# Kernel optimization log

Hardware: AMD Instinct MI355X
Metric: run time of the kernel (lower is better)

Reference implementation:

```python
import jax, jax.numpy as jnp
import numpy as np

B, N, C = 8, 4096, 768
H = 4 * C  # mlp hidden
EPS = 1e-7
LN_EPS = 1e-5


def _ln(x, g, b):
    mu = jnp.mean(x, axis=-1, keepdims=True)
    var = jnp.mean((x - mu) ** 2, axis=-1, keepdims=True)
    return (x - mu) * jax.lax.rsqrt(var + LN_EPS) * g + b


def _mlp(z, w1, b1, w2, b2):
    return jax.nn.gelu(z @ w1 + b1, approximate=False) @ w2 + b2


def setup_inputs() -> dict:
    key = jax.random.key(0)
    ks = jax.random.split(key, 16)
    s = 1.0 / np.sqrt(C)
    inp = {
        "x": jax.random.normal(ks[0], (B, N, C), jnp.float32),
        "y": jax.random.normal(ks[1], (B, N, C), jnp.float32),
        "mask": jax.random.randint(ks[2], (B, N, 1), 0, 2).astype(jnp.float32),
        "h": 64,
        "w": 64,
        "ln1_g": jnp.ones((C,), jnp.float32),
        "ln1_b": jnp.zeros((C,), jnp.float32),
        "Wq": jax.random.normal(ks[3], (C, C), jnp.float32) * s,
        "Wk": jax.random.normal(ks[4], (C, C), jnp.float32) * s,
        "Wv": jax.random.normal(ks[5], (C, C), jnp.float32) * s,
        "Wpx": jax.random.normal(ks[6], (2 * C, C), jnp.float32) * s,
        "Wpy": jax.random.normal(ks[7], (2 * C, C), jnp.float32) * s,
        "ln2_g": jnp.ones((C,), jnp.float32),
        "ln2_b": jnp.zeros((C,), jnp.float32),
        "fx1_w": jax.random.normal(ks[8], (C, H), jnp.float32) * s,
        "fx1_b": jnp.zeros((H,), jnp.float32),
        "fx2_w": jax.random.normal(ks[9], (H, C), jnp.float32) / np.sqrt(H),
        "fx2_b": jnp.zeros((C,), jnp.float32),
        "fy1_w": jax.random.normal(ks[10], (C, H), jnp.float32) * s,
        "fy1_b": jnp.zeros((H,), jnp.float32),
        "fy2_w": jax.random.normal(ks[11], (H, C), jnp.float32) / np.sqrt(H),
        "fy2_b": jnp.zeros((C,), jnp.float32),
    }
    return inp


def _minmax(s):
    mn = jnp.min(s, axis=1, keepdims=True)
    mx = jnp.max(s, axis=1, keepdims=True)
    return (s - mn) / (mx - mn + EPS)


def reference(x, y, mask, h, w, ln1_g, ln1_b, Wq, Wk, Wv, Wpx, Wpy,
              ln2_g, ln2_b, fx1_w, fx1_b, fx2_w, fx2_b, fy1_w, fy1_b, fy2_w, fy2_b):
    b, n, c = x.shape
    m = mask.reshape(b, n, 1)  # binary mask per token
    xn = _ln(x, ln1_g, ln1_b)
    yn = _ln(y, ln1_g, ln1_b)
    q = yn @ Wq  # (b,n,c)
    k = xn @ Wk
    v = xn @ Wv
    # masked GAP pools (Weighted_GAP): (b,c)
    fg = jnp.sum(q * m, axis=1) / (jnp.sum(m, axis=1) + 5e-4)
    bg = jnp.sum(q * (1.0 - m), axis=1) / (jnp.sum(1.0 - m, axis=1) + 5e-4)
    k_nrm = jnp.linalg.norm(k, axis=2)  # (b,n)
    fg_nrm = jnp.linalg.norm(fg, axis=1, keepdims=True)  # (b,1)
    bg_nrm = jnp.linalg.norm(bg, axis=1, keepdims=True)
    fg_s = jnp.einsum('bnc,bc->bn', k, fg) / (k_nrm * fg_nrm + EPS)
    bg_s = jnp.einsum('bnc,bc->bn', k, bg) / (k_nrm * bg_nrm + EPS)
    scores = _minmax(fg_s) - _minmax(bg_s)  # (b,n)
    pseudo_mask = scores.reshape(b, 1, h, w)
    attn = jax.nn.softmax(jnp.where(scores < 0, scores - 100.0, scores), axis=1)
    query_pro = jnp.einsum('bn,bnc->bc', attn, v)  # (b,c)
    qp_nrm = jnp.linalg.norm(query_pro, axis=1, keepdims=True)
    sim = jnp.sum(query_pro * fg, axis=1, keepdims=True) / (qp_nrm * fg_nrm + EPS)
    sim = (sim + 1.0) * 0.5  # (b,1)
    pro = sim * fg + (1.0 - sim) * query_pro  # (b,c)
    pro_b = jnp.broadcast_to(pro[:, None, :], x.shape)
    xo = x + jnp.concatenate([x, pro_b], axis=-1) @ Wpx
    yo = y + jnp.concatenate([y, pro_b], axis=-1) @ Wpy
    xo = xo + _mlp(_ln(xo, ln2_g, ln2_b), fx1_w, fx1_b, fx2_w, fx2_b)
    yo = yo + _mlp(_ln(yo, ln2_g, ln2_b), fy1_w, fy1_b, fy2_w, fy2_b)
    return (xo, yo, pseudo_mask)
```

## Files before the change

### kernel.cpp

```cpp
#include <hip/hip_runtime.h>
#include <math.h>

#define B_ 8
#define N_ 4096
#define C_ 768
#define H_ 3072
#define M_ (B_*N_)
#define NSPLIT 16

typedef unsigned short u16;
typedef unsigned int u32;
typedef __attribute__((ext_vector_type(8))) __bf16 bf16x8;
typedef __attribute__((ext_vector_type(4))) float f32x4;
typedef __attribute__((ext_vector_type(4))) unsigned short u16x4;
typedef __attribute__((ext_vector_type(8))) unsigned short u16x8;

__device__ __forceinline__ u16 f2bf(float f){
  u32 u = __float_as_uint(f);
  u32 r = (u + 0x7FFFu + ((u >> 16) & 1u)) >> 16;
  return (u16)r;
}
__device__ __forceinline__ float bf2f(u16 h){
  return __uint_as_float(((u32)h) << 16);
}
__device__ __forceinline__ void gload_lds16(const void* g, void* l){
  __builtin_amdgcn_global_load_lds((const __attribute__((address_space(1))) void*)g,
                                   (__attribute__((address_space(3))) void*)l, 16, 0, 0);
}

template<int EPI, int GM>
__global__ __launch_bounds__(512, 4) void gemm_bf16(
    const u16* __restrict__ A, const u16* __restrict__ BT,
    int K, int N, int NBN,
    void* __restrict__ outp,
    const float* __restrict__ resid,
    const float* __restrict__ rowv,
    const float* __restrict__ bias)
{
  __shared__ u16 lds[3][12288];
  const int tid = threadIdx.x;
  const int wid = tid >> 6, lane = tid & 63;

  const int nwg = gridDim.x;
  int wg = blockIdx.x;
  wg = (wg & 7) * (nwg >> 3) + (wg >> 3);
  const int GMN = GM * NBN;
  const int g = wg / GMN, r = wg % GMN;
  const int bm = (g*GM + (r % GM)) * 256;
  const int bn = (r / GM) * 128;

  const int wr = wid >> 1, wc = wid & 1;
  const int l15 = lane & 15;

  f32x4 acc[4][4];
#pragma unroll
  for (int i=0;i<4;i++)
#pragma unroll
    for (int j=0;j<4;j++) acc[i][j] = (f32x4){0.f,0.f,0.f,0.f};

  const int srow = tid >> 2;
  const int lchq = (tid & 3) ^ ((tid >> 3) & 3);
  const u16* agp0 = A  + (size_t)(bm + srow)*K       + lchq*8;
  const u16* agp1 = A  + (size_t)(bm + 128 + srow)*K + lchq*8;
  const u16* bgp0 = BT + (size_t)(bn + srow)*K       + lchq*8;

  auto STAGE = [&](int bi){
    char* base = (char*)lds[bi] + wid*1024;
    gload_lds16(agp0, base);
    gload_lds16(agp1, base + 8192);
    gload_lds16(bgp0, base + 16384);
    agp0 += 32; agp1 += 32; bgp0 += 32;
  };

  const int arow = wr*64 + l15;
  const int brow = wc*64 + l15;
  const int aswz = (arow >> 1) & 3;
  const int bswz = (brow >> 1) & 3;
  const int aoff = arow*32 + (((lane>>4) ^ aswz) << 3);
  const int boff = 8192 + brow*32 + (((lane>>4) ^ bswz) << 3);

  const int nk = K >> 5;
  STAGE(0);
  STAGE(1);
  int kk2 = 0;

#define KSTEP(BI) do {                                                        \
    if (kk2 == nk-1){ asm volatile("s_waitcnt vmcnt(0)" ::: "memory"); }      \
    else            { asm volatile("s_waitcnt vmcnt(3)" ::: "memory"); }      \
    __builtin_amdgcn_s_barrier();                                             \
    __builtin_amdgcn_sched_barrier(0);                                        \
    if (kk2+2 < nk) STAGE((BI)==0 ? 2 : (BI)-1);            \
    bf16x8 av[4], bv[4];                                                      \
    const u16* pa = &lds[BI][aoff];                                           \
    const u16* pb = &lds[BI][boff];                                           \
    _Pragma("unroll")                                                         \
    for (int i=0;i<4;i++){                                                    \
      av[i] = *reinterpret_cast<const bf16x8*>(pa + i*512);                   \
      bv[i] = *reinterpret_cast<const bf16x8*>(pb + i*512);                   \
    }                                                                         \
    _Pragma("unroll")                                                         \
    for (int i=0;i<4;i++)                                                     \
      _Pragma("unroll")                                                       \
      for (int j=0;j<4;j++)                                                   \
        acc[i][j] = __builtin_amdgcn_mfma_f32_16x16x32_bf16(av[i], bv[j],     \
                                                            acc[i][j],0,0,0); \
    kk2++;                                                                    \
  } while(0)

  for (int it = 0; it < nk/3; it++){
    KSTEP(0);
    KSTEP(1);
    KSTEP(2);
  }
#undef KSTEP

  const int col0 = bn + wc*64 + l15;
  const int row0 = bm + wr*64 + ((lane >> 4) << 2);
#pragma unroll
  for (int i=0;i<4;i++){
#pragma unroll
    for (int j=0;j<4;j++){
#pragma unroll
      for (int r2=0;r2<4;r2++){
        const int row = row0 + i*16 + r2;
        const int cj  = col0 + j*16;
        const size_t o = (size_t)row*N + cj;
        const float va = acc[i][j][r2];
        if constexpr (EPI == 0){
          ((u16*)outp)[o] = f2bf(va);
        } else if constexpr (EPI == 1){
          const float rs = __builtin_nontemporal_load(resid + o);
          ((float*)outp)[o] = rs + va + rowv[(row >> 12)*N + cj];
        } else if constexpr (EPI == 2){
          const float z = va + bias[cj];
          ((u16*)outp)[o] = f2bf(0.5f*z*(1.0f + erff(z*0.70710678f)));
        } else {
          float* po = (float*)outp + o;
          const float prev = __builtin_nontemporal_load(po);
          *po = prev + va + bias[cj];
        }
      }
    }
  }
}

__device__ __forceinline__ void ln_row(const float* __restrict__ p,
    const float* __restrict__ gam, const float* __restrict__ bet,
    u16* __restrict__ op, int lane)
{
  float4 v0 = *reinterpret_cast<const float4*>(p + lane*4);
  float4 v1 = *reinterpret_cast<const float4*>(p + lane*4 + 256);
  float4 v2 = *reinterpret_cast<const float4*>(p + lane*4 + 512);
  float s  = v0.x+v0.y+v0.z+v0.w + v1.x+v1.y+v1.z+v1.w + v2.x+v2.y+v2.z+v2.w;
  float sq = v0.x*v0.x+v0.y*v0.y+v0.z*v0.z+v0.w*v0.w
           + v1.x*v1.x+v1.y*v1.y+v1.z*v1.z+v1.w*v1.w
           + v2.x*v2.x+v2.y*v2.y+v2.z*v2.z+v2.w*v2.w;
#pragma unroll
  for (int o=32;o>0;o>>=1){ s += __shfl_xor(s,o); sq += __shfl_xor(sq,o); }
  const float mu = s * (1.f/C_);
  const float rs = rsqrtf(sq*(1.f/C_) - mu*mu + 1e-5f);
  float4 g0 = *reinterpret_cast<const float4*>(gam + lane*4);
  float4 g1 = *reinterpret_cast<const float4*>(gam + lane*4 + 256);
  float4 g2 = *reinterpret_cast<const float4*>(gam + lane*4 + 512);
  float4 b0 = *reinterpret_cast<const float4*>(bet + lane*4);
  float4 b1 = *reinterpret_cast<const float4*>(bet + lane*4 + 256);
  float4 b2 = *reinterpret_cast<const float4*>(bet + lane*4 + 512);
  u16x4 o0, o1, o2;
  o0[0]=f2bf((v0.x-mu)*rs*g0.x+b0.x); o0[1]=f2bf((v0.y-mu)*rs*g0.y+b0.y);
  o0[2]=f2bf((v0.z-mu)*rs*g0.z+b0.z); o0[3]=f2bf((v0.w-mu)*rs*g0.w+b0.w);
  o1[0]=f2bf((v1.x-mu)*rs*g1.x+b1.x); o1[1]=f2bf((v1.y-mu)*rs*g1.y+b1.y);
  o1[2]=f2bf((v1.z-mu)*rs*g1.z+b1.z); o1[3]=f2bf((v1.w-mu)*rs*g1.w+b1.w);
  o2[0]=f2bf((v2.x-mu)*rs*g2.x+b2.x); o2[1]=f2bf((v2.y-mu)*rs*g2.y+b2.y);
  o2[2]=f2bf((v2.z-mu)*rs*g2.z+b2.z); o2[3]=f2bf((v2.w-mu)*rs*g2.w+b2.w);
  *reinterpret_cast<u16x4*>(op + lane*4)       = o0;
  *reinterpret_cast<u16x4*>(op + lane*4 + 256) = o1;
  *reinterpret_cast<u16x4*>(op + lane*4 + 512) = o2;
}

__global__ __launch_bounds__(256) void ln_fwd(const float* __restrict__ in,
    const float* __restrict__ gam, const float* __restrict__ bet,
    u16* __restrict__ out)
{
  const int row  = blockIdx.x*4 + (threadIdx.x >> 6);
  const int lane = threadIdx.x & 63;
  ln_row(in + (size_t)row*C_, gam, bet, out + (size_t)row*C_, lane);
}

__global__ __launch_bounds__(256) void ln_fwd2(const float* __restrict__ inx,
    const float* __restrict__ iny, const float* __restrict__ gam,
    const float* __restrict__ bet, u16* __restrict__ outx, u16* __restrict__ outy,
    u16* __restrict__ outxb, u16* __restrict__ outyb)
{
  const int row  = blockIdx.x*4 + (threadIdx.x >> 6);
  const int lane = threadIdx.x & 63;
  const float* in = blockIdx.y ? iny : inx;
  u16* out  = blockIdx.y ? outy  : outx;
  u16* outb = blockIdx.y ? outyb : outxb;
  const float* p = in + (size_t)row*C_;
  u16* op  = out  + (size_t)row*C_;
  u16* opb = outb + (size_t)row*C_;

  float4 v0 = *reinterpret_cast<const float4*>(p + lane*4);
  float4 v1 = *reinterpret_cast<const float4*>(p + lane*4 + 256);
  float4 v2 = *reinterpret_cast<const float4*>(p + lane*4 + 512);
  u16x4 rb;
  rb[0]=f2bf(v0.x); rb[1]=f2bf(v0.y); rb[2]=f2bf(v0.z); rb[3]=f2bf(v0.w);
  *reinterpret_cast<u16x4*>(opb + lane*4) = rb;
  rb[0]=f2bf(v1.x); rb[1]=f2bf(v1.y); rb[2]=f2bf(v1.z); rb[3]=f2bf(v1.w);
  *reinterpret_cast<u16x4*>(opb + lane*4 + 256) = rb;
  rb[0]=f2bf(v2.x); rb[1]=f2bf(v2.y); rb[2]=f2bf(v2.z); rb[3]=f2bf(v2.w);
  *reinterpret_cast<u16x4*>(opb + lane*4 + 512) = rb;

  float s  = v0.x+v0.y+v0.z+v0.w + v1.x+v1.y+v1.z+v1.w + v2.x+v2.y+v2.z+v2.w;
  float sq = v0.x*v0.x+v0.y*v0.y+v0.z*v0.z+v0.w*v0.w
           + v1.x*v1.x+v1.y*v1.y+v1.z*v1.z+v1.w*v1.w
           + v2.x*v2.x+v2.y*v2.y+v2.z*v2.z+v2.w*v2.w;
#pragma unroll
  for (int o=32;o>0;o>>=1){ s += __shfl_xor(s,o); sq += __shfl_xor(sq,o); }
  const float mu = s * (1.f/C_);
  const float rs = rsqrtf(sq*(1.f/C_) - mu*mu + 1e-5f);
  float4 g0 = *reinterpret_cast<const float4*>(gam + lane*4);
  float4 g1 = *reinterpret_cast<const float4*>(gam + lane*4 + 256);
  float4 g2 = *reinterpret_cast<const float4*>(gam + lane*4 + 512);
  float4 b0 = *reinterpret_cast<const float4*>(bet + lane*4);
  float4 b1 = *reinterpret_cast<const float4*>(bet + lane*4 + 256);
  float4 b2 = *reinterpret_cast<const float4*>(bet + lane*4 + 512);
  u16x4 o0, o1, o2;
  o0[0]=f2bf((v0.x-mu)*rs*g0.x+b0.x); o0[1]=f2bf((v0.y-mu)*rs*g0.y+b0.y);
  o0[2]=f2bf((v0.z-mu)*rs*g0.z+b0.z); o0[3]=f2bf((v0.w-mu)*rs*g0.w+b0.w);
  o1[0]=f2bf((v1.x-mu)*rs*g1.x+b1.x); o1[1]=f2bf((v1.y-mu)*rs*g1.y+b1.y);
  o1[2]=f2bf((v1.z-mu)*rs*g1.z+b1.z); o1[3]=f2bf((v1.w-mu)*rs*g1.w+b1.w);
  o2[0]=f2bf((v2.x-mu)*rs*g2.x+b2.x); o2[1]=f2bf((v2.y-mu)*rs*g2.y+b2.y);
  o2[2]=f2bf((v2.z-mu)*rs*g2.z+b2.z); o2[3]=f2bf((v2.w-mu)*rs*g2.w+b2.w);
  *reinterpret_cast<u16x4*>(op + lane*4)       = o0;
  *reinterpret_cast<u16x4*>(op + lane*4 + 256) = o1;
  *reinterpret_cast<u16x4*>(op + lane*4 + 512) = o2;
}

__device__ __forceinline__ void tr_tile(const float* __restrict__ in,
    u16* __restrict__ outp, int R, int Cc, int t)
{
  __shared__ float tile[32][33];
  const int tilesx = Cc >> 5;
  const int c0 = (t % tilesx)*32, r0 = (t / tilesx)*32;
  const int tx = threadIdx.x & 31, ty = threadIdx.x >> 5;
#pragma unroll
  for (int i=0;i<32;i+=8)
    tile[ty+i][tx] = in[(size_t)(r0+ty+i)*Cc + c0+tx];
  __syncthreads();
#pragma unroll
  for (int i=0;i<32;i+=8)
    outp[(size_t)(c0+ty+i)*R + r0+tx] = f2bf(tile[tx][ty+i]);
}

__global__ __launch_bounds__(256) void transpose_all(
    const float* Wk, const float* Wpx, const float* Wpy,
    const float* f1x, const float* f2x, const float* f1y, const float* f2y,
    u16* WkT, u16* WpxT, u16* WpyT, u16* f1xT, u16* f2xT, u16* f1yT, u16* f2yT)
{
  int t = blockIdx.x;
  if (t < 1728){
    const int m = t / 576; t -= m*576;
    const float* in = (m==0)?Wk:((m==1)?Wpx:Wpy);
    u16* o = (m==0)?WkT:((m==1)?WpxT:WpyT);
    tr_tile(in, o, C_, C_, t);
  } else {
    t -= 1728;
    const int m = t / 2304; t -= m*2304;
    if (m==0)      tr_tile(f1x, f1xT, C_, H_, t);
    else if (m==1) tr_tile(f2x, f2xT, H_, C_, t);
    else if (m==2) tr_tile(f1y, f1yT, C_, H_, t);
    else           tr_tile(f2y, f2yT, H_, C_, t);
  }
}

__global__ __launch_bounds__(256) void pool_partial(const u16* __restrict__ q,
    const float* __restrict__ mask, float* __restrict__ pm, float* __restrict__ pa,
    float* __restrict__ mpart)
{
  const int c = blockIdx.x*256 + threadIdx.x;
  const int b = blockIdx.y, z = blockIdx.z;
  const int n0 = z*(N_/NSPLIT);
  const u16* qp = q + ((size_t)b*N_ + n0)*C_ + c;
  const float* mp = mask + (size_t)b*N_ + n0;
  float am=0.f, aa=0.f, ms=0.f;
  for (int n=0;n<N_/NSPLIT;n++){
    float v = bf2f(qp[(size_t)n*C_]);
    float m = mp[n];
    am += v*m; aa += v; ms += m;
  }
  const size_t o = ((size_t)z*B_ + b)*C_ + c;
  pm[o]=am; pa[o]=aa;
  if (blockIdx.x==0 && threadIdx.x==0) mpart[z*B_+b] = ms;
}

__global__ __launch_bounds__(256) void proto_fused(const float* __restrict__ pm,
    const float* __restrict__ pa, const float* __restrict__ mpart,
    const float* __restrict__ Wq,
    float* __restrict__ fg, float* __restrict__ bg,
    float* __restrict__ fgn, float* __restrict__ bgn)
{
  __shared__ float fin[C_], bin[C_];
  __shared__ float red[8];
  const int b = blockIdx.x, tid = threadIdx.x;
  float msum_b = 0.f;
#pragma unroll
  for (int z=0;z<NSPLIT;z++) msum_b += mpart[z*B_+b];
  for (int c=tid;c<C_;c+=256){
    float sm=0.f, sa=0.f;
#pragma unroll
    for (int z=0;z<NSPLIT;z++){ size_t o=((size_t)z*B_+b)*C_+c; sm+=pm[o]; sa+=pa[o]; }
    fin[c] = sm/(msum_b + 5e-4f);
    bin[c] = (sa - sm)/((float)N_ - msum_b + 5e-4f);
  }
  __syncthreads();
  const int j0 = tid, j1 = tid+256, j2 = tid+512;
  float f0=0,f1=0,f2=0,g0=0,g1=0,g2=0;
  for (int c=0;c<C_;c++){
    const float* w = Wq + (size_t)c*C_;
    float fc = fin[c], bc = bin[c];
    float w0=w[j0], w1=w[j1], w2=w[j2];
    f0 += fc*w0; f1 += fc*w1; f2 += fc*w2;
    g0 += bc*w0; g1 += bc*w1; g2 += bc*w2;
  }
  fg[b*C_+j0]=f0; fg[b*C_+j1]=f1; fg[b*C_+j2]=f2;
  bg[b*C_+j0]=g0; bg[b*C_+j1]=g1; bg[b*C_+j2]=g2;
  float sf = f0*f0+f1*f1+f2*f2, sb = g0*g0+g1*g1+g2*g2;
#pragma unroll
  for (int o=32;o>0;o>>=1){ sf+=__shfl_down(sf,o); sb+=__shfl_down(sb,o); }
  if ((tid&63)==0){ red[tid>>6]=sf; red[4+(tid>>6)]=sb; }
  __syncthreads();
  if (tid==0){
    fgn[b]=sqrtf(red[0]+red[1]+red[2]+red[3]);
    bgn[b]=sqrtf(red[4]+red[5]+red[6]+red[7]);
  }
}

__global__ __launch_bounds__(256) void score_kernel(const u16* __restrict__ k,
    const float* __restrict__ fg, const float* __restrict__ bg,
    const float* __restrict__ fgn, const float* __restrict__ bgn,
    float* __restrict__ fg_s, float* __restrict__ bg_s)
{
  const int t = blockIdx.x*4 + (threadIdx.x >> 6);
  const int lane = threadIdx.x & 63;
  const int b = t >> 12;
  const u16* kp = k + (size_t)t*C_;
  u16x8 k8 = *reinterpret_cast<const u16x8*>(kp + lane*8);
  u16x4 k4 = *reinterpret_cast<const u16x4*>(kp + 512 + lane*4);
  const float* fgp = fg + b*C_;
  const float* bgp = bg + b*C_;
  float4 fa = *reinterpret_cast<const float4*>(fgp + lane*8);
  float4 fb = *reinterpret_cast<const float4*>(fgp + lane*8 + 4);
  float4 fc = *reinterpret_cast<const float4*>(fgp + 512 + lane*4);
  float4 ba = *reinterpret_cast<const float4*>(bgp + lane*8);
  float4 bb = *reinterpret_cast<const float4*>(bgp + lane*8 + 4);
  float4 bc = *reinterpret_cast<const float4*>(bgp + 512 + lane*4);
  float kv[12];
#pragma unroll
  for (int i=0;i<8;i++) kv[i] = bf2f(k8[i]);
#pragma unroll
  for (int i=0;i<4;i++) kv[8+i] = bf2f(k4[i]);
  float df = kv[0]*fa.x+kv[1]*fa.y+kv[2]*fa.z+kv[3]*fa.w
           + kv[4]*fb.x+kv[5]*fb.y+kv[6]*fb.z+kv[7]*fb.w
           + kv[8]*fc.x+kv[9]*fc.y+kv[10]*fc.z+kv[11]*fc.w;
  float db = kv[0]*ba.x+kv[1]*ba.y+kv[2]*ba.z+kv[3]*ba.w
           + kv[4]*bb.x+kv[5]*bb.y+kv[6]*bb.z+kv[7]*bb.w
           + kv[8]*bc.x+kv[9]*bc.y+kv[10]*bc.z+kv[11]*bc.w;
  float kk=0.f;
#pragma unroll
  for (int i=0;i<12;i++) kk += kv[i]*kv[i];
#pragma unroll
  for (int o=32;o>0;o>>=1){
    df+=__shfl_xor(df,o); db+=__shfl_xor(db,o); kk+=__shfl_xor(kk,o);
  }
  if (lane==0){
    const float kn = sqrtf(kk);
    fg_s[t] = df/(kn*fgn[b]+1e-7f);
    bg_s[t] = db/(kn*bgn[b]+1e-7f);
  }
}

__global__ __launch_bounds__(256) void minmax_kernel(const float* __restrict__ fg_s,
    const float* __restrict__ bg_s, float* __restrict__ mm)
{
  __shared__ float sm[16];
  const int b = blockIdx.x;
  float mnf=1e30f, mxf=-1e30f, mnb=1e30f, mxb=-1e30f;
  for (int i=threadIdx.x;i<N_;i+=256){
    float a = fg_s[(size_t)b*N_+i]; mnf=fminf(mnf,a); mxf=fmaxf(mxf,a);
    float c = bg_s[(size_t)b*N_+i]; mnb=fminf(mnb,c); mxb=fmaxf(mxb,c);
  }
#pragma unroll
  for (int o=32;o>0;o>>=1){
    mnf=fminf(mnf,__shfl_down(mnf,o)); mxf=fmaxf(mxf,__shfl_down(mxf,o));
    mnb=fminf(mnb,__shfl_down(mnb,o)); mxb=fmaxf(mxb,__shfl_down(mxb,o));
  }
  const int wid = threadIdx.x>>6;
  if ((threadIdx.x&63)==0){ sm[wid]=mnf; sm[4+wid]=mxf; sm[8+wid]=mnb; sm[12+wid]=mxb; }
  __syncthreads();
  if (threadIdx.x==0){
    mm[b*4+0]=fminf(fminf(sm[0],sm[1]),fminf(sm[2],sm[3]));
    mm[b*4+1]=fmaxf(fmaxf(sm[4],sm[5]),fmaxf(sm[6],sm[7]));
    mm[b*4+2]=fminf(fminf(sm[8],sm[9]),fminf(sm[10],sm[11]));
    mm[b*4+3]=fmaxf(fmaxf(sm[12],sm[13]),fmaxf(sm[14],sm[15]));
  }
}

__global__ __launch_bounds__(1024) void scorefin_fused(const float* __restrict__ fg_s,
    const float* __restrict__ bg_s, const float* __restrict__ mm,
    float* __restrict__ pseudo, float* __restrict__ escr, float* __restrict__ denom)
{
  __shared__ float sm[16];
  const int b = blockIdx.x, tid = threadIdx.x;
  const float mnf=mm[b*4+0], mxf=mm[b*4+1], mnb=mm[b*4+2], mxb=mm[b*4+3];
  const float rf = 1.f/(mxf-mnf+1e-7f), rb = 1.f/(mxb-mnb+1e-7f);
  float ps = 0.f;
#pragma unroll
  for (int i=0;i<4;i++){
    const int t = tid + i*1024;
    const size_t o = (size_t)b*N_ + t;
    const float s = (fg_s[o]-mnf)*rf - (bg_s[o]-mnb)*rb;
    pseudo[o] = s;
    const float e = expf(s < 0.f ? s - 100.f : s);
    escr[o] = e;
    ps += e;
  }
#pragma unroll
  for (int o=32;o>0;o>>=1) ps += __shfl_down(ps,o);
  if ((tid&63)==0) sm[tid>>6]=ps;
  __syncthreads();
  if (tid==0){
    float s=0.f;
#pragma unroll
    for (int w=0;w<16;w++) s+=sm[w];
    denom[b]=s;
  }
}

__global__ __launch_bounds__(256) void vpool_partial(const u16* __restrict__ xn,
    const float* __restrict__ e, float* __restrict__ pv)
{
  const int c = blockIdx.x*256 + threadIdx.x;
  const int b = blockIdx.y, z = blockIdx.z;
  const int n0 = z*(N_/NSPLIT);
  const u16* vp = xn + ((size_t)b*N_ + n0)*C_ + c;
  const float* ep = e + (size_t)b*N_ + n0;
  float acc=0.f;
  for (int n=0;n<N_/NSPLIT;n++) acc += bf2f(vp[(size_t)n*C_])*ep[n];
  pv[((size_t)z*B_+b)*C_+c] = acc;
}

__global__ __launch_bounds__(256) void pro_fused(const float* __restrict__ pv,
    const float* __restrict__ denom,
    const float* __restrict__ Wv, const float* __restrict__ Wpx,
    const float* __restrict__ Wpy,
    const float* __restrict__ fg, const float* __restrict__ fgn,
    float* __restrict__ rowx, float* __restrict__ rowy)
{
  __shared__ float vin[C_];
  __shared__ float red[8];
  __shared__ float simsh;
  const int b = blockIdx.x, tid = threadIdx.x;
  const float den = 1.f/denom[b];
  for (int c=tid;c<C_;c+=256){
    float s=0.f;
#pragma unroll
    for (int z=0;z<NSPLIT;z++) s += pv[((size_t)z*B_+b)*C_+c];
    vin[c] = s*den;
  }
  __syncthreads();
  const int j0 = tid, j1 = tid+256, j2 = tid+512;
  float q0=0,q1=0,q2=0;
  for (int c=0;c<C_;c++){
    const float* w = Wv + (size_t)c*C_;
    float vv = vin[c];
    q0 += vv*w[j0]; q1 += vv*w[j1]; q2 += vv*w[j2];
  }
  const float fg0 = fg[b*C_+j0], fg1 = fg[b*C_+j1], fg2 = fg[b*C_+j2];
  float d = q0*fg0 + q1*fg1 + q2*fg2;
  float qq = q0*q0 + q1*q1 + q2*q2;
#pragma unroll
  for (int o=32;o>0;o>>=1){ d+=__shfl_down(d,o); qq+=__shfl_down(qq,o); }
  if ((tid&63)==0){ red[tid>>6]=d; red[4+(tid>>6)]=qq; }
  __syncthreads();
  if (tid==0){
    float dd=red[0]+red[1]+red[2]+red[3], qs=red[4]+red[5]+red[6]+red[7];
    simsh = (dd/(sqrtf(qs)*fgn[b]+1e-7f)+1.f)*0.5f;
  }
  __syncthreads();
  const float sim = simsh;
  vin[j0] = sim*fg0 + (1.f-sim)*q0;
  vin[j1] = sim*fg1 + (1.f-sim)*q1;
  vin[j2] = sim*fg2 + (1.f-sim)*q2;
  __syncthreads();
  float rx0=0,rx1=0,rx2=0, ry0=0,ry1=0,ry2=0;
  for (int c=0;c<C_;c++){
    const float* wx = Wpx + (size_t)(C_+c)*C_;
    const float* wy = Wpy + (size_t)(C_+c)*C_;
    float pc = vin[c];
    rx0 += pc*wx[j0]; rx1 += pc*wx[j1]; rx2 += pc*wx[j2];
    ry0 += pc*wy[j0]; ry1 += pc*wy[j1]; ry2 += pc*wy[j2];
  }
  rowx[b*C_+j0]=rx0; rowx[b*C_+j1]=rx1; rowx[b*C_+j2]=rx2;
  rowy[b*C_+j0]=ry0; rowy[b*C_+j1]=ry1; rowy[b*C_+j2]=ry2;
}

extern "C" void kernel_launch(void* const* d_in, const int* in_sizes, int n_in,
                              void* d_out, int out_size, void* d_ws, size_t ws_size,
                              hipStream_t stream)
{
  const float* x     = (const float*)d_in[0];
  const float* y     = (const float*)d_in[1];
  const float* mask  = (const float*)d_in[2];
  const float* ln1_g = (const float*)d_in[5];
  const float* ln1_b = (const float*)d_in[6];
  const float* Wq    = (const float*)d_in[7];
  const float* Wk    = (const float*)d_in[8];
  const float* Wv    = (const float*)d_in[9];
  const float* Wpx   = (const float*)d_in[10];
  const float* Wpy   = (const float*)d_in[11];
  const float* ln2_g = (const float*)d_in[12];
  const float* ln2_b = (const float*)d_in[13];
  const float* fx1_w = (const float*)d_in[14];
  const float* fx1_b = (const float*)d_in[15];
  const float* fx2_w = (const float*)d_in[16];
  const float* fx2_b = (const float*)d_in[17];
  const float* fy1_w = (const float*)d_in[18];
  const float* fy1_b = (const float*)d_in[19];
  const float* fy2_w = (const float*)d_in[20];
  const float* fy2_b = (const float*)d_in[21];

  float* out    = (float*)d_out;
  float* out_xo = out;
  float* out_yo = out + (size_t)M_*C_;
  float* out_ps = out + 2*(size_t)M_*C_;

  char* ws = (char*)d_ws;
  const size_t ACT = (size_t)M_*C_;
  u16* R0  = (u16*)ws;
  u16* xnb = R0;
  u16* ynb = R0 + ACT;
  u16* kb  = R0 + 2*ACT;
  u16* xb  = R0 + 3*ACT;
  u16* yb  = (u16*)(ws + 4*ACT*2);
  u16* qb  = yb;
  u16* hid = R0;
  u16* wp  = (u16*)(ws + 5*ACT*2);
  u16* WkT  = wp;
  u16* WpxT = wp + 1*589824;
  u16* WpyT = wp + 2*589824;
  u16* fx1T = wp + 3*589824;
  u16* fx2T = fx1T + 2359296;
  u16* fy1T = fx2T + 2359296;
  u16* fy2T = fy1T + 2359296;
  float* st   = (float*)(ws + 5*ACT*2 + (size_t)(3*589824 + 4*2359296)*2);
  float* fgn  = st + 8;
  float* bgn  = st + 16;
  float* denom= st + 24;
  float* mm   = st + 32;
  float* fg   = st + 64;
  float* bg   = st + 6208;
  float* rowx = st + 24640;
  float* rowy = st + 30784;
  float* fg_s = st + 37056;
  float* bg_s = st + 69824;
  float* escr = st + 102592;
  float* pm   = st + 135360;
  float* pa   = st + 233664;
  float* pv   = st + 331968;
  float* mpart= st + 430272;

  dim3 tb(256);
  dim3 tg(512);

  transpose_all<<<dim3(10944),tb,0,stream>>>(Wk,Wpx,Wpy,fx1_w,fx2_w,fy1_w,fy2_w,
                                             WkT,WpxT,WpyT,fx1T,fx2T,fy1T,fy2T);
  ln_fwd2<<<dim3(M_/4,2),tb,0,stream>>>(x, y, ln1_g, ln1_b, xnb, ynb, xb, yb);

  gemm_bf16<0,8><<<dim3(128*6),tg,0,stream>>>(xnb, WkT, C_, C_, 6, kb, nullptr,nullptr,nullptr);

  pool_partial<<<dim3(3,B_,NSPLIT),tb,0,stream>>>(ynb, mask, pm, pa, mpart);
  proto_fused<<<B_,tb,0,stream>>>(pm, pa, mpart, Wq, fg, bg, fgn, bgn);

  score_kernel<<<M_/4,tb,0,stream>>>(kb, fg, bg, fgn, bgn, fg_s, bg_s);
  minmax_kernel<<<B_,tb,0,stream>>>(fg_s, bg_s, mm);
  scorefin_fused<<<B_,dim3(1024),0,stream>>>(fg_s, bg_s, mm, out_ps, escr, denom);

  vpool_partial<<<dim3(3,B_,NSPLIT),tb,0,stream>>>(xnb, escr, pv);
  pro_fused<<<B_,tb,0,stream>>>(pv, denom, Wv, Wpx, Wpy, fg, fgn, rowx, rowy);

  gemm_bf16<1,8><<<dim3(128*6),tg,0,stream>>>(xb, WpxT, C_, C_, 6, out_xo, x, rowx, nullptr);
  gemm_bf16<1,8><<<dim3(128*6),tg,0,stream>>>(yb, WpyT, C_, C_, 6, out_yo, y, rowy, nullptr);

  ln_fwd<<<M_/4,tb,0,stream>>>(out_xo, ln2_g, ln2_b, qb);
  gemm_bf16<2,8><<<dim3(128*24),tg,0,stream>>>(qb, fx1T, C_, H_, 24, hid, nullptr,nullptr, fx1_b);
  gemm_bf16<3,2><<<dim3(128*6),tg,0,stream>>>(hid, fx2T, H_, C_, 6, out_xo, nullptr,nullptr, fx2_b);

  ln_fwd<<<M_/4,tb,0,stream>>>(out_yo, ln2_g, ln2_b, qb);
  gemm_bf16<2,8><<<dim3(128*24),tg,0,stream>>>(qb, fy1T, C_, H_, 24, hid, nullptr,nullptr, fy1_b);
  gemm_bf16<3,2><<<dim3(128*6),tg,0,stream>>>(hid, fy2T, H_, C_, 6, out_yo, nullptr,nullptr, fy2_b);
}
```

Baseline: 1.523 ms.

## Replace 256x128 GEMM with 256x256 tile, 8-phase LDS pipeline and setprio

Replaces the bf16 MFMA GEMM with a 256x256 output tile per workgroup. Each wave computes a 128x64 block, and 128KB of LDS is double-buffered over 64-wide K tiles. The K loop is split into eight phases, each interleaving a global-to-LDS stage with LDS reads and 16 MFMAs, using s_setprio to favour the MFMA issue. The goal is to raise arithmetic intensity per byte loaded and hide load latency. In exchange, occupancy drops to 2 blocks per CU, the grid has half as many workgroups, and the grouped-M tile swizzle is removed.

```diff
diff --git a/kernel.cpp b/kernel.cpp
--- a/kernel.cpp
+++ b/kernel.cpp
@@ -28,104 +28,129 @@
                                    (__attribute__((address_space(3))) void*)l, 16, 0, 0);
 }
 
-template<int EPI, int GM>
-__global__ __launch_bounds__(512, 4) void gemm_bf16(
-    const u16* __restrict__ A, const u16* __restrict__ BT,
+
+#define MM4(FM, AV) \
+  acc[FM][0] = __builtin_amdgcn_mfma_f32_16x16x32_bf16(AV, b0, acc[FM][0],0,0,0); \
+  acc[FM][1] = __builtin_amdgcn_mfma_f32_16x16x32_bf16(AV, b1, acc[FM][1],0,0,0); \
+  acc[FM][2] = __builtin_amdgcn_mfma_f32_16x16x32_bf16(AV, b2, acc[FM][2],0,0,0); \
+  acc[FM][3] = __builtin_amdgcn_mfma_f32_16x16x32_bf16(AV, b3, acc[FM][3],0,0,0);
+
+#define STAGE256(H2) do { if ((H2) < Htot){                                  \
+  const int kt_ = (H2)>>2, ty_ = (H2)&3;                                     \
+  const int kh_ = ty_>>1; const int isA_ = ty_&1;                            \
+  const size_t ko_ = (size_t)kt_*64 + (size_t)kh_*32;                        \
+  char* ld_ = ldsc + ((kt_&1)<<16) + ((isA_^1)<<15) + (kh_<<14) + tid*16;    \
+  const u16* g0_ = (isA_ ? Ap + Ab0 : Bp + Bb0) + ko_;                       \
+  const u16* g1_ = (isA_ ? Ap + Ab1 : Bp + Bb1) + ko_;                       \
+  gload_lds16(g0_, ld_);                                                     \
+  gload_lds16(g1_, ld_ + 8192);                                              \
+}} while(0)
+
+#define PHASE(BUFB, KHB, FMQ, LOADB, VMN) do {                               \
+  const u16* pa_ = ldsu + (((BUFB)+(KHB))>>1) + aoffA;                       \
+  bf16x8 a0_ = *(const bf16x8*)(pa_ + ((FMQ)*4+0)*512);                      \
+  bf16x8 a1_ = *(const bf16x8*)(pa_ + ((FMQ)*4+1)*512);                      \
+  bf16x8 a2_ = *(const bf16x8*)(pa_ + ((FMQ)*4+2)*512);                      \
+  bf16x8 a3_ = *(const bf16x8*)(pa_ + ((FMQ)*4+3)*512);                      \
+  if (LOADB){                                                                \
+    const u16* pb_ = ldsu + (((BUFB)+32768+(KHB))>>1) + boffB;               \
+    b0 = *(const bf16x8*)(pb_ + 0*512);                                      \
+    b1 = *(const bf16x8*)(pb_ + 1*512);                                      \
+    b2 = *(const bf16x8*)(pb_ + 2*512);                                      \
+    b3 = *(const bf16x8*)(pb_ + 3*512);                                      \
+  }                                                                          \
+  STAGE256(hh); hh++;                                                        \
+  __builtin_amdgcn_s_barrier();                                              \
+  asm volatile("s_waitcnt lgkmcnt(0)" ::: "memory");                         \
+  __builtin_amdgcn_sched_barrier(0);                                         \
+  __builtin_amdgcn_s_setprio(1);                                             \
+  MM4((FMQ)*4+0, a0_)                                                        \
+  MM4((FMQ)*4+1, a1_)                                                        \
+  MM4((FMQ)*4+2, a2_)                                                        \
+  MM4((FMQ)*4+3, a3_)                                                        \
+  __builtin_amdgcn_s_setprio(0);                                             \
+  if ((VMN) == 6) { asm volatile("s_waitcnt vmcnt(6)" ::: "memory"); }       \
+  else if ((VMN) == 0) { asm volatile("s_waitcnt vmcnt(0)" ::: "memory"); }  \
+  __builtin_amdgcn_s_barrier();                                              \
+} while(0)
+
+template<int EPI>
+__global__ __launch_bounds__(512, 2) void gemm256(
+    const u16* __restrict__ Ap, const u16* __restrict__ Bp,
     int K, int N, int NBN,
     void* __restrict__ outp,
     const float* __restrict__ resid,
     const float* __restrict__ rowv,
     const float* __restrict__ bias)
 {
-  __shared__ u16 lds[3][12288];
+  __shared__ __align__(16) char ldsraw[131072];
+  char* ldsc = ldsraw;
+  const u16* ldsu = (const u16*)ldsraw;
+
   const int tid = threadIdx.x;
   const int wid = tid >> 6, lane = tid & 63;
+  const int wr = wid >> 2, wc = wid & 3;
+  const int l15 = lane & 15;
 
   const int nwg = gridDim.x;
   int wg = blockIdx.x;
   wg = (wg & 7) * (nwg >> 3) + (wg >> 3);
-  const int GMN = GM * NBN;
-  const int g = wg / GMN, r = wg % GMN;
-  const int bm = (g*GM + (r % GM)) * 256;
-  const int bn = (r / GM) * 128;
-
-  const int wr = wid >> 1, wc = wid & 1;
-  const int l15 = lane & 15;
-
-  f32x4 acc[4][4];
-#pragma unroll
-  for (int i=0;i<4;i++)
+  const int bm = (wg / NBN) * 256;
+  const int bn = (wg % NBN) * 256;
+
+  f32x4 acc[8][4];
+#pragma unroll
+  for (int i=0;i<8;i++)
 #pragma unroll
     for (int j=0;j<4;j++) acc[i][j] = (f32x4){0.f,0.f,0.f,0.f};
 
-  const int srow = tid >> 2;
-  const int lchq = (tid & 3) ^ ((tid >> 3) & 3);
-  const u16* agp0 = A  + (size_t)(bm + srow)*K       + lchq*8;
-  const u16* agp1 = A  + (size_t)(bm + 128 + srow)*K + lchq*8;
-  const u16* bgp0 = BT + (size_t)(bn + srow)*K       + lchq*8;
-
-  auto STAGE = [&](int bi){
-    char* base = (char*)lds[bi] + wid*1024;
-    gload_lds16(agp0, base);
-    gload_lds16(agp1, base + 8192);
-    gload_lds16(bgp0, base + 16384);
-    agp0 += 32; agp1 += 32; bgp0 += 32;
-  };
-
-  const int arow = wr*64 + l15;
-  const int brow = wc*64 + l15;
-  const int aswz = (arow >> 1) & 3;
-  const int bswz = (brow >> 1) & 3;
-  const int aoff = arow*32 + (((lane>>4) ^ aswz) << 3);
-  const int boff = 8192 + brow*32 + (((lane>>4) ^ bswz) << 3);
-
-  const int nk = K >> 5;
-  STAGE(0);
-  STAGE(1);
-  int kk2 = 0;
-
-#define KSTEP(BI) do {                                                        \
-    if (kk2 == nk-1){ asm volatile("s_waitcnt vmcnt(0)" ::: "memory"); }      \
-    else            { asm volatile("s_waitcnt vmcnt(3)" ::: "memory"); }      \
-    __builtin_amdgcn_s_barrier();                                             \
-    __builtin_amdgcn_sched_barrier(0);                                        \
-    if (kk2+2 < nk) STAGE((BI)==0 ? 2 : (BI)-1);            \
-    bf16x8 av[4], bv[4];                                                      \
-    const u16* pa = &lds[BI][aoff];                                           \
-    const u16* pb = &lds[BI][boff];                                           \
-    _Pragma("unroll")                                                         \
-    for (int i=0;i<4;i++){                                                    \
-      av[i] = *reinterpret_cast<const bf16x8*>(pa + i*512);                   \
-      bv[i] = *reinterpret_cast<const bf16x8*>(pb + i*512);                   \
-    }                                                                         \
-    _Pragma("unroll")                                                         \
-    for (int i=0;i<4;i++)                                                     \
-      _Pragma("unroll")                                                       \
-      for (int j=0;j<4;j++)                                                   \
-        acc[i][j] = __builtin_amdgcn_mfma_f32_16x16x32_bf16(av[i], bv[j],     \
-                                                            acc[i][j],0,0,0); \
-    kk2++;                                                                    \
-  } while(0)
-
-  for (int it = 0; it < nk/3; it++){
-    KSTEP(0);
-    KSTEP(1);
-    KSTEP(2);
-  }
-#undef KSTEP
+  const int r0s = tid >> 2, c0s = (tid & 3) ^ ((tid >> 3) & 3);
+  const size_t Ab0 = (size_t)(bm + r0s)*K       + (size_t)c0s*8;
+  const size_t Ab1 = (size_t)(bm + 128 + r0s)*K + (size_t)c0s*8;
+  const size_t Bb0 = (size_t)(bn + r0s)*K       + (size_t)c0s*8;
+  const size_t Bb1 = (size_t)(bn + 128 + r0s)*K + (size_t)c0s*8;
+
+  const int physcb = ((lane >> 4) << 4) ^ (((l15 >> 1) & 3) << 4);
+  const int aoffA = (wr*128 + l15)*32 + (physcb >> 1);
+  const int boffB = (wc*64  + l15)*32 + (physcb >> 1);
+
+  const int T = K >> 6;
+  const int Htot = T*4;
+  bf16x8 b0, b1, b2, b3;
+
+  int hh = 0;
+  STAGE256(0); STAGE256(1); STAGE256(2); STAGE256(3);
+  asm volatile("s_waitcnt vmcnt(4)" ::: "memory");
+  STAGE256(4); STAGE256(5); STAGE256(6);
+  asm volatile("s_waitcnt vmcnt(6)" ::: "memory");
+  __builtin_amdgcn_s_barrier();
+  hh = 7;
+
+  for (int kt = 0; kt < T; kt += 2){
+    const int vm4 = (kt+1 == T-1) ? 0 : 6;
+    const int vm8 = (kt+2 >= T) ? -1 : 6;
+    PHASE(0,     0,     0, 1, -1);
+    PHASE(0,     0,     1, 0, -1);
+    PHASE(0,     16384, 0, 1, -1);
+    PHASE(0,     16384, 1, 0, vm4);
+    PHASE(65536, 0,     0, 1, -1);
+    PHASE(65536, 0,     1, 0, -1);
+    PHASE(65536, 16384, 0, 1, -1);
+    PHASE(65536, 16384, 1, 0, vm8);
+  }
 
   const int col0 = bn + wc*64 + l15;
-  const int row0 = bm + wr*64 + ((lane >> 4) << 2);
-#pragma unroll
-  for (int i=0;i<4;i++){
-#pragma unroll
-    for (int j=0;j<4;j++){
-#pragma unroll
-      for (int r2=0;r2<4;r2++){
-        const int row = row0 + i*16 + r2;
-        const int cj  = col0 + j*16;
+  const int row0 = bm + wr*128 + ((lane >> 4) << 2);
+#pragma unroll
+  for (int fm=0; fm<8; fm++){
+#pragma unroll
+    for (int fn=0; fn<4; fn++){
+#pragma unroll
+      for (int r2=0; r2<4; r2++){
+        const int row = row0 + fm*16 + r2;
+        const int cj  = col0 + fn*16;
         const size_t o = (size_t)row*N + cj;
-        const float va = acc[i][j][r2];
+        const float va = acc[fm][fn][r2];
         if constexpr (EPI == 0){
           ((u16*)outp)[o] = f2bf(va);
         } else if constexpr (EPI == 1){
@@ -577,7 +602,7 @@
                                              WkT,WpxT,WpyT,fx1T,fx2T,fy1T,fy2T);
   ln_fwd2<<<dim3(M_/4,2),tb,0,stream>>>(x, y, ln1_g, ln1_b, xnb, ynb, xb, yb);
 
-  gemm_bf16<0,8><<<dim3(128*6),tg,0,stream>>>(xnb, WkT, C_, C_, 6, kb, nullptr,nullptr,nullptr);
+  gemm256<0><<<dim3(128*3),tg,0,stream>>>(xnb, WkT, C_, C_, 3, kb, nullptr,nullptr,nullptr);
 
   pool_partial<<<dim3(3,B_,NSPLIT),tb,0,stream>>>(ynb, mask, pm, pa, mpart);
   proto_fused<<<B_,tb,0,stream>>>(pm, pa, mpart, Wq, fg, bg, fgn, bgn);
@@ -589,14 +614,14 @@
   vpool_partial<<<dim3(3,B_,NSPLIT),tb,0,stream>>>(xnb, escr, pv);
   pro_fused<<<B_,tb,0,stream>>>(pv, denom, Wv, Wpx, Wpy, fg, fgn, rowx, rowy);
 
-  gemm_bf16<1,8><<<dim3(128*6),tg,0,stream>>>(xb, WpxT, C_, C_, 6, out_xo, x, rowx, nullptr);
-  gemm_bf16<1,8><<<dim3(128*6),tg,0,stream>>>(yb, WpyT, C_, C_, 6, out_yo, y, rowy, nullptr);
+  gemm256<1><<<dim3(128*3),tg,0,stream>>>(xb, WpxT, C_, C_, 3, out_xo, x, rowx, nullptr);
+  gemm256<1><<<dim3(128*3),tg,0,stream>>>(yb, WpyT, C_, C_, 3, out_yo, y, rowy, nullptr);
 
   ln_fwd<<<M_/4,tb,0,stream>>>(out_xo, ln2_g, ln2_b, qb);
-  gemm_bf16<2,8><<<dim3(128*24),tg,0,stream>>>(qb, fx1T, C_, H_, 24, hid, nullptr,nullptr, fx1_b);
-  gemm_bf16<3,2><<<dim3(128*6),tg,0,stream>>>(hid, fx2T, H_, C_, 6, out_xo, nullptr,nullptr, fx2_b);
+  gemm256<2><<<dim3(128*12),tg,0,stream>>>(qb, fx1T, C_, H_, 12, hid, nullptr,nullptr, fx1_b);
+  gemm256<3><<<dim3(128*3),tg,0,stream>>>(hid, fx2T, H_, C_, 3, out_xo, nullptr,nullptr, fx2_b);
 
   ln_fwd<<<M_/4,tb,0,stream>>>(out_yo, ln2_g, ln2_b, qb);
-  gemm_bf16<2,8><<<dim3(128*24),tg,0,stream>>>(qb, fy1T, C_, H_, 24, hid, nullptr,nullptr, fy1_b);
-  gemm_bf16<3,2><<<dim3(128*6),tg,0,stream>>>(hid, fy2T, H_, C_, 6, out_yo, nullptr,nullptr, fy2_b);
-}
+  gemm256<2><<<dim3(128*12),tg,0,stream>>>(qb, fy1T, C_, H_, 12, hid, nullptr,nullptr, fy1_b);
+  gemm256<3><<<dim3(128*3),tg,0,stream>>>(hid, fy2T, H_, C_, 3, out_yo, nullptr,nullptr, fy2_b);
+}
```

New measurement: 1.754 ms. 15.1% more time.
